# Kernel tuning notes

Measured on AMD Instinct MI355X. Metric: run time of the kernel, lower is better.

The kernel has to match this reference:

```python
import jax, jax.numpy as jnp
import numpy as np

B = 256          # batch of images
TOK = 256        # 16x16 tokens per image
V = 1024         # codebook size
D = 256          # code dim


def setup_inputs() -> dict:
    key = jax.random.key(0)
    k1, k2, k3, k4 = jax.random.split(key, 4)
    image_seq = jax.random.randint(k1, (B, TOK), 0, V, dtype=jnp.int64)
    image_seq2 = jax.random.randint(k2, (B, TOK), 0, V, dtype=jnp.int64)
    alpha = jax.random.uniform(k3, (1,), dtype=jnp.float32)
    W = jax.random.normal(k4, (V, D), dtype=jnp.float32)
    return {"image_seq": image_seq, "image_seq2": image_seq2, "alpha": alpha, "W": W}


def reference(image_seq, image_seq2, alpha, W):
    a = alpha[0]
    # gather codebook entries: [B, TOK, D]
    emb = W[image_seq]
    emb2 = W[image_seq2]
    x = (1.0 - a) * emb + a * emb2
    xf = x.reshape(-1, D)                        # [N, D], N = B*TOK
    # brute-force L2 distance to every code, without materializing [N, V, D]:
    d = (jnp.sum(xf * xf, axis=-1, keepdims=True)
         - 2.0 * xf @ W.T
         + jnp.sum(W * W, axis=-1)[None, :])
    idx = jnp.argmin(d, axis=1)                  # top-1 nearest code, [N]
    # get_codebook_entry: gather, reshape to bhwc, permute to bchw
    z_q = W[idx].reshape(B, 16, 16, D)           # [B, 16, 16, 256]
    z_q = jnp.transpose(z_q, (0, 3, 1, 2))       # [B, 256, 16, 16]
    return z_q
```

## Files before the change

kernel.cpp:

```cpp
#include <hip/hip_runtime.h>

static constexpr int Vn = 1024;
static constexpr int Dn = 256;
static constexpr int NT = 65536;

__global__ __launch_bounds__(256) void gram_kernel(const float* __restrict__ W,
                                                   float* __restrict__ G) {
    __shared__ float As[16][65];
    __shared__ float Bs[16][65];
    const int tid = threadIdx.x;
    const int tx = tid & 15;
    const int ty = tid >> 4;
    const int bm = blockIdx.y * 64;
    const int bn = blockIdx.x * 64;
    float acc[4][4] = {};
    for (int k0 = 0; k0 < Dn; k0 += 16) {
#pragma unroll
        for (int s = 0; s < 4; ++s) {
            int e = tid + 256 * s;
            int m = e >> 4;
            int k = e & 15;
            As[k][m] = W[(bm + m) * Dn + k0 + k];
            Bs[k][m] = W[(bn + m) * Dn + k0 + k];
        }
        __syncthreads();
#pragma unroll
        for (int kk = 0; kk < 16; ++kk) {
            float a[4], b[4];
#pragma unroll
            for (int u = 0; u < 4; ++u) a[u] = As[kk][ty * 4 + u];
#pragma unroll
            for (int u = 0; u < 4; ++u) b[u] = Bs[kk][tx * 4 + u];
#pragma unroll
            for (int u = 0; u < 4; ++u)
#pragma unroll
                for (int w = 0; w < 4; ++w)
                    acc[u][w] = fmaf(a[u], b[w], acc[u][w]);
        }
        __syncthreads();
    }
#pragma unroll
    for (int u = 0; u < 4; ++u) {
        const int row = bm + ty * 4 + u;
#pragma unroll
        for (int w = 0; w < 4; ++w) {
            G[row * Vn + bn + tx * 4 + w] = acc[u][w];
        }
    }
}

__global__ void diag_kernel(const float* __restrict__ G, float* __restrict__ norms) {
    const int v = blockIdx.x * 256 + threadIdx.x;
    norms[v] = G[v * (Vn + 1)];
}

__global__ __launch_bounds__(256) void argmin_kernel(const int* __restrict__ seq,
                                                     const int* __restrict__ seq2,
                                                     const float* __restrict__ alpha,
                                                     const float* __restrict__ G,
                                                     const float* __restrict__ norms,
                                                     int* __restrict__ out_idx) {
    __shared__ float nrm[Vn];
    const int tid = threadIdx.x;
    {
        const float4* n4 = (const float4*)norms;
        float4* s4 = (float4*)nrm;
        s4[tid] = n4[tid];
    }
    __syncthreads();
    const float a = alpha[0];
    const float c0 = -2.0f * (1.0f - a);
    const float c1 = -2.0f * a;
    const int wave = tid >> 6;
    const int lane = tid & 63;
    const int base_t = blockIdx.x * 16 + wave * 4;
    const float4* nr = (const float4*)nrm;
    for (int q = 0; q < 4; ++q) {
        const int t = base_t + q;
        const int i = seq[t];
        const int j = seq2[t];
        const float4* Gi = (const float4*)(G + i * Vn);
        const float4* Gj = (const float4*)(G + j * Vn);
        float best = __builtin_inff();
        int bestV = 0;
#pragma unroll
        for (int s = 0; s < 4; ++s) {
            const int e = s * 64 + lane;
            const float4 gi = Gi[e];
            const float4 gj = Gj[e];
            const float4 nn = nr[e];
            const float sc0 = fmaf(c1, gj.x, fmaf(c0, gi.x, nn.x));
            const float sc1 = fmaf(c1, gj.y, fmaf(c0, gi.y, nn.y));
            const float sc2 = fmaf(c1, gj.z, fmaf(c0, gi.z, nn.z));
            const float sc3 = fmaf(c1, gj.w, fmaf(c0, gi.w, nn.w));
            const int v = e * 4;
            if (sc0 < best) { best = sc0; bestV = v; }
            if (sc1 < best) { best = sc1; bestV = v + 1; }
            if (sc2 < best) { best = sc2; bestV = v + 2; }
            if (sc3 < best) { best = sc3; bestV = v + 3; }
        }
#pragma unroll
        for (int off = 32; off >= 1; off >>= 1) {
            const float ob = __shfl_down(best, off, 64);
            const int   ov = __shfl_down(bestV, off, 64);
            if (ob < best || (ob == best && ov < bestV)) { best = ob; bestV = ov; }
        }
        if (lane == 0) out_idx[t] = bestV;
    }
}

__global__ __launch_bounds__(256) void gather_transpose_kernel(const float* __restrict__ W,
                                                               const int* __restrict__ idx,
                                                               float* __restrict__ out) {
    __shared__ float tile[32][33];
    const int b   = blockIdx.z;
    const int hw0 = blockIdx.x * 32;
    const int d0  = blockIdx.y * 32;
    const int tx  = threadIdx.x & 31;
    const int ty  = threadIdx.x >> 5;
#pragma unroll
    for (int r = ty; r < 32; r += 8) {
        const int row = idx[b * 256 + hw0 + r];
        tile[r][tx] = W[row * Dn + d0 + tx];
    }
    __syncthreads();
#pragma unroll
    for (int r = ty; r < 32; r += 8) {
        out[b * 65536 + (d0 + r) * 256 + hw0 + tx] = tile[tx][r];
    }
}

extern "C" void kernel_launch(void* const* d_in, const int* in_sizes, int n_in,
                              void* d_out, int out_size, void* d_ws, size_t ws_size,
                              hipStream_t stream) {
    const int*   seq   = (const int*)d_in[0];
    const int*   seq2  = (const int*)d_in[1];
    const float* alpha = (const float*)d_in[2];
    const float* W     = (const float*)d_in[3];
    float* out = (float*)d_out;

    char* ws = (char*)d_ws;
    float* G     = (float*)ws;
    float* norms = (float*)(ws + (size_t)Vn * Vn * 4);
    int*   idx   = (int*)(ws + (size_t)Vn * Vn * 4 + Vn * 4);

    gram_kernel<<<dim3(16, 16), 256, 0, stream>>>(W, G);
    diag_kernel<<<Vn / 256, 256, 0, stream>>>(G, norms);
    argmin_kernel<<<NT / 16, 256, 0, stream>>>(seq, seq2, alpha, G, norms, idx);
    gather_transpose_kernel<<<dim3(8, 8, 256), 256, 0, stream>>>(W, idx, out);
}
```

Measured before the change: 145.7 us.

## Bucket tokens by first code index and reuse precomputed Gram row per block

Adds a counting sort (histogram, scan, scatter) that groups tokens by their first codebook index. Each argmin block then handles one code i, folds norms and the -2(1-a)·G[i] term into shared memory once, and streams only G[j] rows per token. It also retiles the Gram kernel into 32x32 blocks that write the diagonal norms directly, which removes the separate diag kernel. The cost is three extra small launches plus atomics and a memset, and load imbalance because bucket sizes vary across blocks.

Result: slower. 183.4 us (+25.9%).

```diff
diff --git a/kernel.cpp b/kernel.cpp
--- a/kernel.cpp
+++ b/kernel.cpp
@@ -5,94 +5,130 @@
 static constexpr int NT = 65536;
 
 __global__ __launch_bounds__(256) void gram_kernel(const float* __restrict__ W,
-                                                   float* __restrict__ G) {
-    __shared__ float As[16][65];
-    __shared__ float Bs[16][65];
+                                                   float* __restrict__ G,
+                                                   float* __restrict__ norms) {
+    __shared__ float As[32][33];
+    __shared__ float Bs[32][33];
     const int tid = threadIdx.x;
     const int tx = tid & 15;
     const int ty = tid >> 4;
-    const int bm = blockIdx.y * 64;
-    const int bn = blockIdx.x * 64;
-    float acc[4][4] = {};
-    for (int k0 = 0; k0 < Dn; k0 += 16) {
+    const int bm = blockIdx.y * 32;
+    const int bn = blockIdx.x * 32;
+    float acc[2][2] = {};
+    for (int k0 = 0; k0 < Dn; k0 += 32) {
 #pragma unroll
         for (int s = 0; s < 4; ++s) {
-            int e = tid + 256 * s;
-            int m = e >> 4;
-            int k = e & 15;
+            const int e = tid + 256 * s;
+            const int m = e >> 5;
+            const int k = e & 31;
             As[k][m] = W[(bm + m) * Dn + k0 + k];
             Bs[k][m] = W[(bn + m) * Dn + k0 + k];
         }
         __syncthreads();
 #pragma unroll
-        for (int kk = 0; kk < 16; ++kk) {
-            float a[4], b[4];
+        for (int kk = 0; kk < 32; ++kk) {
+            float a[2], b[2];
 #pragma unroll
-            for (int u = 0; u < 4; ++u) a[u] = As[kk][ty * 4 + u];
+            for (int u = 0; u < 2; ++u) a[u] = As[kk][ty + 16 * u];
 #pragma unroll
-            for (int u = 0; u < 4; ++u) b[u] = Bs[kk][tx * 4 + u];
+            for (int w = 0; w < 2; ++w) b[w] = Bs[kk][tx + 16 * w];
 #pragma unroll
-            for (int u = 0; u < 4; ++u)
+            for (int u = 0; u < 2; ++u)
 #pragma unroll
-                for (int w = 0; w < 4; ++w)
+                for (int w = 0; w < 2; ++w)
                     acc[u][w] = fmaf(a[u], b[w], acc[u][w]);
         }
         __syncthreads();
     }
 #pragma unroll
-    for (int u = 0; u < 4; ++u) {
-        const int row = bm + ty * 4 + u;
+    for (int u = 0; u < 2; ++u) {
+        const int row = bm + ty + 16 * u;
 #pragma unroll
-        for (int w = 0; w < 4; ++w) {
-            G[row * Vn + bn + tx * 4 + w] = acc[u][w];
+        for (int w = 0; w < 2; ++w) {
+            const int col = bn + tx + 16 * w;
+            G[row * Vn + col] = acc[u][w];
+            if (row == col) norms[row] = acc[u][w];
         }
     }
 }
 
-__global__ void diag_kernel(const float* __restrict__ G, float* __restrict__ norms) {
-    const int v = blockIdx.x * 256 + threadIdx.x;
-    norms[v] = G[v * (Vn + 1)];
+__global__ void hist_kernel(const int* __restrict__ seq, int* __restrict__ counts) {
+    const int t = blockIdx.x * 256 + threadIdx.x;
+    atomicAdd(&counts[seq[t]], 1);
 }
 
-__global__ __launch_bounds__(256) void argmin_kernel(const int* __restrict__ seq,
-                                                     const int* __restrict__ seq2,
+__global__ __launch_bounds__(1024) void scan_kernel(const int* __restrict__ counts,
+                                                    int* __restrict__ base,
+                                                    int* __restrict__ cursor) {
+    __shared__ int sc[1024];
+    const int tid = threadIdx.x;
+    const int c = counts[tid];
+    sc[tid] = c;
+    __syncthreads();
+    for (int off = 1; off < 1024; off <<= 1) {
+        int v = sc[tid];
+        if (tid >= off) v += sc[tid - off];
+        __syncthreads();
+        sc[tid] = v;
+        __syncthreads();
+    }
+    const int b = sc[tid] - c;
+    base[tid] = b;
+    cursor[tid] = b;
+    if (tid == 1023) base[1024] = sc[1023];
+}
+
+__global__ void scatter_kernel(const int* __restrict__ seq, int* __restrict__ cursor,
+                               int* __restrict__ sorted) {
+    const int t = blockIdx.x * 256 + threadIdx.x;
+    const int p = atomicAdd(&cursor[seq[t]], 1);
+    sorted[p] = t;
+}
+
+__global__ __launch_bounds__(256) void argmin_kernel(const int* __restrict__ seq2,
                                                      const float* __restrict__ alpha,
                                                      const float* __restrict__ G,
                                                      const float* __restrict__ norms,
+                                                     const int* __restrict__ base,
+                                                     const int* __restrict__ sorted,
                                                      int* __restrict__ out_idx) {
-    __shared__ float nrm[Vn];
+    __shared__ float s[Vn];
+    const int i = blockIdx.x;
     const int tid = threadIdx.x;
-    {
-        const float4* n4 = (const float4*)norms;
-        float4* s4 = (float4*)nrm;
-        s4[tid] = n4[tid];
-    }
-    __syncthreads();
     const float a = alpha[0];
     const float c0 = -2.0f * (1.0f - a);
     const float c1 = -2.0f * a;
+    {
+        const float4 g = ((const float4*)(G + i * Vn))[tid];
+        const float4 n = ((const float4*)norms)[tid];
+        float4 r;
+        r.x = fmaf(c0, g.x, n.x);
+        r.y = fmaf(c0, g.y, n.y);
+        r.z = fmaf(c0, g.z, n.z);
+        r.w = fmaf(c0, g.w, n.w);
+        ((float4*)s)[tid] = r;
+    }
+    __syncthreads();
+    const int start = base[i];
+    const int end = base[i + 1];
     const int wave = tid >> 6;
     const int lane = tid & 63;
-    const int base_t = blockIdx.x * 16 + wave * 4;
-    const float4* nr = (const float4*)nrm;
-    for (int q = 0; q < 4; ++q) {
-        const int t = base_t + q;
-        const int i = seq[t];
+    const float4* s4 = (const float4*)s;
+    for (int p = start + wave; p < end; p += 4) {
+        const int t = sorted[p];
         const int j = seq2[t];
-        const float4* Gi = (const float4*)(G + i * Vn);
         const float4* Gj = (const float4*)(G + j * Vn);
         float best = __builtin_inff();
         int bestV = 0;
 #pragma unroll
-        for (int s = 0; s < 4; ++s) {
-            const int e = s * 64 + lane;
-            const float4 gi = Gi[e];
+        for (int q = 0; q < 4; ++q) {
+            const int e = q * 64 + lane;
             const float4 gj = Gj[e];
-            const float4 nn = nr[e];
-            const float sc0 = fmaf(c1, gj.x, fmaf(c0, gi.x, nn.x));
-            const float sc1 = fmaf(c1, gj.y, fmaf(c0, gi.y, nn.y));
-            const float sc2 = fmaf(c1, gj.z, fmaf(c0, gi.z, nn.z));
-            const float sc3 = fmaf(c1, gj.w, fmaf(c0, gi.w, nn.w));
+            const float4 ss = s4[e];
+            const float sc0 = fmaf(c1, gj.x, ss.x);
+            const float sc1 = fmaf(c1, gj.y, ss.y);
+            const float sc2 = fmaf(c1, gj.z, ss.z);
+            const float sc3 = fmaf(c1, gj.w, ss.w);
             const int v = e * 4;
             if (sc0 < best) { best = sc0; bestV = v; }
             if (sc1 < best) { best = sc1; bestV = v + 1; }
@@ -140,12 +176,19 @@
     float* out = (float*)d_out;
 
     char* ws = (char*)d_ws;
-    float* G     = (float*)ws;
-    float* norms = (float*)(ws + (size_t)Vn * Vn * 4);
-    int*   idx   = (int*)(ws + (size_t)Vn * Vn * 4 + Vn * 4);
+    float* G      = (float*)(ws);
+    float* norms  = (float*)(ws + 4194304);
+    int*   idx    = (int*)  (ws + 4198400);
+    int*   counts = (int*)  (ws + 4460544);
+    int*   base   = (int*)  (ws + 4464640);
+    int*   cursor = (int*)  (ws + 4468752);
+    int*   sorted = (int*)  (ws + 4472848);
 
-    gram_kernel<<<dim3(16, 16), 256, 0, stream>>>(W, G);
-    diag_kernel<<<Vn / 256, 256, 0, stream>>>(G, norms);
-    argmin_kernel<<<NT / 16, 256, 0, stream>>>(seq, seq2, alpha, G, norms, idx);
+    gram_kernel<<<dim3(32, 32), 256, 0, stream>>>(W, G, norms);
+    hipMemsetAsync(counts, 0, Vn * sizeof(int), stream);
+    hist_kernel<<<NT / 256, 256, 0, stream>>>(seq, counts);
+    scan_kernel<<<1, 1024, 0, stream>>>(counts, base, cursor);
+    scatter_kernel<<<NT / 256, 256, 0, stream>>>(seq, cursor, sorted);
+    argmin_kernel<<<Vn, 256, 0, stream>>>(seq2, alpha, G, norms, base, sorted, idx);
     gather_transpose_kernel<<<dim3(8, 8, 256), 256, 0, stream>>>(W, idx, out);
 }
```
